# Optimization experiments

Measured on AMD Instinct MI355X. Metric: run time of the kernel, lower is better.

Reference implementation:

```python
import jax, jax.numpy as jnp
import numpy as np
from jax import lax

TWN_THRESHOLD_FACTOR = 0.05
BN_EPS = 1e-5


@jax.custom_vjp
def _ternary_quant(w, t):
    return (w > t).astype(w.dtype) - (w < -t).astype(w.dtype)

def _tq_fwd(w, t):
    mask = (w > t) | (w < -t)
    return _ternary_quant(w, t), mask

def _tq_bwd(mask, g):
    return (g * mask.astype(g.dtype), jnp.zeros((), g.dtype))

_ternary_quant.defvjp(_tq_fwd, _tq_bwd)


def quantize(w):
    # threshold is detached in the original (weight.detach().abs().max())
    t = TWN_THRESHOLD_FACTOR * jnp.max(jnp.abs(lax.stop_gradient(w)))
    return _ternary_quant(w, t)


def conv2d(x, w, b):
    # x: [N,C,H,W], w: [O,I,K,K], valid conv, stride 1
    y = lax.conv_general_dilated(x, w, (1, 1), 'VALID',
                                 dimension_numbers=('NCHW', 'OIHW', 'NCHW'))
    return y + b[None, :, None, None]


def maxpool2(x):
    return lax.reduce_window(x, -jnp.inf, lax.max,
                             (1, 1, 2, 2), (1, 1, 2, 2), 'VALID')


def bn2d(x, g, b):
    # training-mode batch norm over (N,H,W), biased variance
    m = jnp.mean(x, (0, 2, 3), keepdims=True)
    v = jnp.mean(jnp.square(x - m), (0, 2, 3), keepdims=True)
    return (x - m) * lax.rsqrt(v + BN_EPS) * g[None, :, None, None] + b[None, :, None, None]


def bn1d(x, g, b):
    m = jnp.mean(x, 0, keepdims=True)
    v = jnp.mean(jnp.square(x - m), 0, keepdims=True)
    return (x - m) * lax.rsqrt(v + BN_EPS) * g[None, :] + b[None, :]


def setup_inputs() -> dict:
    key = jax.random.key(0)
    ks = jax.random.split(key, 12)
    N = 4096
    inp = {
        'x': jax.random.normal(ks[0], (N, 1, 28, 28), jnp.float32),
        'w1': jax.random.normal(ks[1], (32, 1, 5, 5), jnp.float32) * 0.2,
        'b1': jnp.zeros((32,), jnp.float32),
        'g1': jnp.ones((32,), jnp.float32),
        'be1': jnp.zeros((32,), jnp.float32),
        'w2': jax.random.normal(ks[2], (64, 32, 5, 5), jnp.float32) * 0.05,
        'b2': jnp.zeros((64,), jnp.float32),
        'g2': jnp.ones((64,), jnp.float32),
        'be2': jnp.zeros((64,), jnp.float32),
        'wf1': jax.random.normal(ks[3], (512, 1024), jnp.float32) * 0.03,
        'bf1': jnp.zeros((512,), jnp.float32),
        'g3': jnp.ones((512,), jnp.float32),
        'be3': jnp.zeros((512,), jnp.float32),
        'wf2': jax.random.normal(ks[4], (10, 512), jnp.float32) * 0.04,
        'bf2': jnp.zeros((10,), jnp.float32),
    }
    return inp


def reference(x, w1, b1, g1, be1, w2, b2, g2, be2, wf1, bf1, g3, be3, wf2, bf2):
    h = jax.nn.relu(bn2d(conv2d(x, quantize(w1), b1), g1, be1))     # [N,32,24,24]
    h = maxpool2(h)                                                  # [N,32,12,12]
    h = jax.nn.relu(bn2d(conv2d(h, quantize(w2), b2), g2, be2))     # [N,64,8,8]
    h = maxpool2(h)                                                  # [N,64,4,4]
    h = h.reshape(h.shape[0], -1)                                    # [N,1024]
    h = jax.nn.relu(bn1d(h @ quantize(wf1).T + bf1, g3, be3))       # [N,512]
    return h @ quantize(wf2).T + bf2                                 # [N,10]
```

## Files before the change

kernel.cpp:

```cpp
#include <hip/hip_runtime.h>

#define TID ((int)threadIdx.x)
typedef unsigned short u16;
typedef short short8 __attribute__((ext_vector_type(8)));
typedef float f32x4 __attribute__((ext_vector_type(4)));
typedef float v2f __attribute__((ext_vector_type(2)));

__device__ __forceinline__ u16 f2b(float f) {
    unsigned int x = __float_as_uint(f);
    return (u16)((x + 0x7fffu + ((x >> 16) & 1u)) >> 16);
}
__device__ __forceinline__ float b2f(u16 u) {
    return __uint_as_float(((unsigned int)u) << 16);
}
__device__ __forceinline__ v2f fma2(float a, v2f b, v2f c) {
    v2f av = {a, a};
    return __builtin_elementwise_fma(av, b, c);
}

static constexpr size_t OFF_QW1   = 0;
static constexpr size_t OFF_QWF2  = 3200;
static constexpr size_t OFF_TMAX  = 23680;
static constexpr size_t OFF_SUM1C = 23808;
static constexpr size_t OFF_SSQ1C = 24832;
static constexpr size_t OFF_SUM2  = 25856, OFF_SSQ2 = 26112;
static constexpr size_t OFF_SUM3  = 26368, OFF_SSQ3 = 28416;
static constexpr size_t STATS_BEG = 23680, STATS_END = 30464;
static constexpr size_t OFF_QW2C  = 30720;
static constexpr size_t OFF_QWF1C = 133120;
static constexpr size_t OFF_Y1P   = 1181696;
static constexpr size_t OFF_Y2C   = 38930432;
static constexpr size_t OFF_H2C   = 72484864;
static constexpr size_t OFF_Y3    = 80873472;

__global__ __launch_bounds__(256) void absmax_k(const float* w1, const float* w2,
                                                const float* wf1, const float* wf2,
                                                unsigned int* tmaxbits) {
    int bid = blockIdx.x;
    int b, lb, nb; const float* src; long n;
    if (bid < 1)        { b = 0; src = w1;  n = 800;    lb = bid;       nb = 1;   }
    else if (bid < 9)   { b = 1; src = w2;  n = 51200;  lb = bid - 1;   nb = 8;   }
    else if (bid < 265) { b = 2; src = wf1; n = 524288; lb = bid - 9;   nb = 256; }
    else                { b = 3; src = wf2; n = 5120;   lb = bid - 265; nb = 1;   }
    float m = 0.f;
    for (long i = (long)lb * 256 + TID; i < n; i += (long)nb * 256)
        m = fmaxf(m, fabsf(src[i]));
    __shared__ float red[256];
    red[TID] = m; __syncthreads();
    for (int s = 128; s > 0; s >>= 1) {
        if (TID < s) red[TID] = fmaxf(red[TID], red[TID + s]);
        __syncthreads();
    }
    if (TID == 0) atomicMax(&tmaxbits[b], __float_as_uint(red[0]));
}

__global__ __launch_bounds__(256) void quant_all_k(const float* w1, const float* w2,
                                                   const float* wf1, const float* wf2,
                                                   float* qw1, u16* qw2c, u16* qwf1c,
                                                   float* qwf2, const unsigned int* tmax) {
    int bid = blockIdx.x;
    if (bid < 4) {
        int i = bid * 256 + TID; if (i >= 800) return;
        float t = 0.05f * __uint_as_float(tmax[0]);
        float v = w1[i];
        qw1[i] = (v > t) ? 1.f : ((v < -t) ? -1.f : 0.f);
    } else if (bid < 204) {
        int i = (bid - 4) * 256 + TID;
        float t = 0.05f * __uint_as_float(tmax[1]);
        int ic = i & 31, oc = (i >> 5) & 63, sh = i >> 11;
        float v = w2[(oc * 32 + ic) * 25 + sh];
        qw2c[i] = f2b((v > t) ? 1.f : ((v < -t) ? -1.f : 0.f));
    } else if (bid < 2252) {
        int i = (bid - 204) * 256 + TID;
        float t = 0.05f * __uint_as_float(tmax[2]);
        float v = wf1[i];
        qwf1c[i] = f2b((v > t) ? 1.f : ((v < -t) ? -1.f : 0.f));
    } else {
        int i = (bid - 2252) * 256 + TID;
        float t = 0.05f * __uint_as_float(tmax[3]);
        float v = wf2[i];
        qwf2[i] = (v > t) ? 1.f : ((v < -t) ? -1.f : 0.f);
    }
}

__global__ __launch_bounds__(256) void conv1_fused_k(const float* __restrict__ x,
                                                     const float* __restrict__ qw1,
                                                     u16* __restrict__ y1p,
                                                     float* sum1c, float* ssq1c) {
    __shared__ float wl[800];
    __shared__ float red[4][64];
    for (int i = TID; i < 800; i += 256) wl[i] = qw1[i];
    __syncthreads();
    int p = blockIdx.x * 256 + TID;
    int cg = p & 15, half = (p >> 4) & 1;
    int pr = p >> 5;
    int py = pr % 12, n = pr / 12;
    int l = TID & 63, wv = TID >> 6;
    const float* xb = x + n * 784 + (2 * py) * 28 + half * 12;
    float patch[6][16];
    #pragma unroll
    for (int r = 0; r < 6; r++) {
        const float4* rp = reinterpret_cast<const float4*>(xb + r * 28);
        #pragma unroll
        for (int qq = 0; qq < 4; qq++) {
            float4 v = rp[qq];
            patch[r][qq * 4 + 0] = v.x; patch[r][qq * 4 + 1] = v.y;
            patch[r][qq * 4 + 2] = v.z; patch[r][qq * 4 + 3] = v.w;
        }
    }
    int c0 = cg * 2;
    v2f wp[25];
    #pragma unroll
    for (int k = 0; k < 25; k++)
        wp[k] = (v2f){wl[c0 * 25 + k], wl[(c0 + 1) * 25 + k]};
    v2f A0[12], A1[12];
    #pragma unroll
    for (int ox = 0; ox < 12; ox++) { A0[ox] = (v2f){0.f, 0.f}; A1[ox] = (v2f){0.f, 0.f}; }
    #pragma unroll
    for (int ky = 0; ky < 5; ky++)
        #pragma unroll
        for (int kx = 0; kx < 5; kx++) {
            v2f w = wp[ky * 5 + kx];
            #pragma unroll
            for (int ox = 0; ox < 12; ox++) {
                A0[ox] = fma2(patch[ky][ox + kx], w, A0[ox]);
                A1[ox] = fma2(patch[ky + 1][ox + kx], w, A1[ox]);
            }
        }
    v2f sv = {0.f, 0.f}, qv = {0.f, 0.f};
    #pragma unroll
    for (int ox = 0; ox < 12; ox++) {
        sv += A0[ox] + A1[ox];
        qv = __builtin_elementwise_fma(A0[ox], A0[ox], qv);
        qv = __builtin_elementwise_fma(A1[ox], A1[ox], qv);
    }
    float st[4] = {sv.x, sv.y, qv.x, qv.y};
    u16* base = y1p + (size_t)n * 4608 + (py * 12 + half * 6) * 32 + c0;
    #pragma unroll
    for (int j = 0; j < 6; j++) {
        v2f pm = __builtin_elementwise_max(
                     __builtin_elementwise_max(A0[2 * j], A0[2 * j + 1]),
                     __builtin_elementwise_max(A1[2 * j], A1[2 * j + 1]));
        unsigned int u = (unsigned int)f2b(pm.x) | ((unsigned int)f2b(pm.y) << 16);
        *reinterpret_cast<unsigned int*>(base + j * 32) = u;
    }
    #pragma unroll
    for (int t = 0; t < 4; t++) {
        st[t] += __shfl_xor(st[t], 16);
        st[t] += __shfl_xor(st[t], 32);
    }
    if (l < 16) {
        #pragma unroll
        for (int t = 0; t < 4; t++) red[wv][l * 4 + t] = st[t];
    }
    __syncthreads();
    if (TID < 64) {
        float v = red[0][TID] + red[1][TID] + red[2][TID] + red[3][TID];
        int t = TID & 3, ch = (TID >> 2) * 2 + (t & 1);
        float* dst = (t < 2 ? sum1c : ssq1c) + (blockIdx.x & 7) * 32 + ch;
        atomicAdd(dst, v);
    }
}

__global__ __launch_bounds__(256) void conv2_k(const u16* __restrict__ y1p,
                                               const u16* __restrict__ qw2c,
                                               u16* __restrict__ y2c,
                                               const float* sum1c, const float* ssq1c,
                                               const float* g1, const float* be1,
                                               float* sum, float* ssq) {
    __shared__ float4 hsm4[1176];
    __shared__ float scs[32], shs[32];
    char* hsraw = (char*)hsm4;
    int n0 = blockIdx.x * 8;
    int l = TID & 63, wv = TID >> 6;
    int oc0 = wv * 16;
    int lm = l & 15, lr = (l >> 3) & 1, ox = l & 7, bq = l >> 4;
    if (TID < 32) {
        float s = 0.f, q = 0.f;
        #pragma unroll
        for (int r = 0; r < 8; r++) { s += sum1c[r * 32 + TID]; q += ssq1c[r * 32 + TID]; }
        float m = s * (1.f / 2359296.f);
        float v = q * (1.f / 2359296.f) - m * m;
        float sc = g1[TID] / sqrtf(v + 1e-5f);
        scs[TID] = sc; shs[TID] = be1[TID] - m * sc;
    }
    __syncthreads();
    float scR[8], shR[8];
    {
        int b = TID & 3;
        #pragma unroll
        for (int j = 0; j < 8; j++) { scR[j] = scs[b * 8 + j]; shR[j] = shs[b * 8 + j]; }
    }
    short8 bw[25];
    #pragma unroll
    for (int sh = 0; sh < 25; sh++)
        bw[sh] = *reinterpret_cast<const short8*>(qw2c + ((size_t)sh * 64 + oc0 + lm) * 32 + bq * 8);
    int xy[5];
    #pragma unroll
    for (int kx = 0; kx < 5; kx++) {
        int xx = ox + kx;
        xy[kx] = lr * 784 + xx * 64 + (((bq + (xx >> 1)) & 3) * 16);
    }
    float sacc = 0.f, s2acc = 0.f;
    {
        const uint4* src = reinterpret_cast<const uint4*>(y1p + (size_t)n0 * 4608);
        #pragma unroll
        for (int k = 0; k < 3; k++) {
            if (k < 2 || TID < 64) {
                int i = TID + k * 256;
                int pix = i >> 2, b = i & 3;
                int y = pix / 12, xx = pix - y * 12;
                union { uint4 v; u16 u[8]; } in, out;
                in.v = src[i];
                #pragma unroll
                for (int j = 0; j < 8; j++)
                    out.u[j] = f2b(fmaxf(fmaf(b2f(in.u[j]), scR[j], shR[j]), 0.f));
                *reinterpret_cast<uint4*>(hsraw + y * 784 + xx * 64 + (((b + (xx >> 1)) & 3) * 16)) = out.v;
            }
        }
    }
    #pragma unroll 1
    for (int s = 0; s < 8; s++) {
        __syncthreads();
        if (s < 7) {
            const uint4* src = reinterpret_cast<const uint4*>(y1p + (size_t)(n0 + s + 1) * 4608);
            char* dst = hsraw + ((s + 1) & 1) * 9408;
            #pragma unroll
            for (int k = 0; k < 3; k++) {
                if (k < 2 || TID < 64) {
                    int i = TID + k * 256;
                    int pix = i >> 2, b = i & 3;
                    int y = pix / 12, xx = pix - y * 12;
                    union { uint4 v; u16 u[8]; } in, out;
                    in.v = src[i];
                    #pragma unroll
                    for (int j = 0; j < 8; j++)
                        out.u[j] = f2b(fmaxf(fmaf(b2f(in.u[j]), scR[j], shR[j]), 0.f));
                    *reinterpret_cast<uint4*>(dst + y * 784 + xx * 64 + (((b + (xx >> 1)) & 3) * 16)) = out.v;
                }
            }
        }
        const char* hb = hsraw + (s & 1) * 9408;
        f32x4 acc[4] = {{0.f,0.f,0.f,0.f},{0.f,0.f,0.f,0.f},{0.f,0.f,0.f,0.f},{0.f,0.f,0.f,0.f}};
        #pragma unroll
        for (int R = 0; R <= 10; R++) {
            short8 a[5];
            #pragma unroll
            for (int kx = 0; kx < 5; kx++)
                a[kx] = *reinterpret_cast<const short8*>(hb + xy[kx] + R * 784);
            #pragma unroll
            for (int mt = 0; mt < 4; mt++) {
                int ky = R - 2 * mt;
                if (ky < 0 || ky > 4) continue;
                #pragma unroll
                for (int kx = 0; kx < 5; kx++)
                    acc[mt] = __builtin_amdgcn_mfma_f32_16x16x32_bf16(a[kx], bw[ky * 5 + kx], acc[mt], 0, 0, 0);
            }
        }
        int n = n0 + s;
        #pragma unroll
        for (int mt = 0; mt < 4; mt++) {
            float v0 = acc[mt][0], v1 = acc[mt][1], v2 = acc[mt][2], v3 = acc[mt][3];
            sacc += v0 + v1 + v2 + v3;
            s2acc += v0 * v0 + v1 * v1 + v2 * v2 + v3 * v3;
            ushort4 u = make_ushort4(f2b(v0), f2b(v1), f2b(v2), f2b(v3));
            *reinterpret_cast<ushort4*>(y2c + (size_t)n * 4096 + (oc0 + lm) * 64 + mt * 16 + bq * 4) = u;
        }
    }
    sacc  += __shfl_xor(sacc, 16);  sacc  += __shfl_xor(sacc, 32);
    s2acc += __shfl_xor(s2acc, 16); s2acc += __shfl_xor(s2acc, 32);
    if (l < 16) { atomicAdd(&sum[oc0 + l], sacc); atomicAdd(&ssq[oc0 + l], s2acc); }
}

__global__ __launch_bounds__(256) void pool2_k(const u16* __restrict__ y2c,
                                               const float* sum2, const float* ssq2,
                                               const float* g2, const float* be2,
                                               u16* __restrict__ h2c) {
    int i = blockIdx.x * 256 + TID;
    int px = i & 3, py = (i >> 2) & 3, oc = (i >> 4) & 63, n = i >> 10;
    float m = sum2[oc] * (1.f / 262144.f);
    float v = ssq2[oc] * (1.f / 262144.f) - m * m;
    float s = g2[oc] / sqrtf(v + 1e-5f);
    float t = be2[oc] - m * s;
    size_t base = (size_t)n * 4096 + oc * 64 + (2 * py) * 8 + 2 * px;
    unsigned int u0 = *reinterpret_cast<const unsigned int*>(y2c + base);
    unsigned int u1 = *reinterpret_cast<const unsigned int*>(y2c + base + 8);
    float a = b2f((u16)u0) * s + t, b = b2f((u16)(u0 >> 16)) * s + t;
    float c = b2f((u16)u1) * s + t, d = b2f((u16)(u1 >> 16)) * s + t;
    float mm = fmaxf(fmaxf(fmaxf(fmaxf(0.f, a), b), c), d);
    h2c[i] = f2b(mm);
}

__global__ __launch_bounds__(256) void fc1_k(const u16* __restrict__ h2c,
                                             const u16* __restrict__ qwf1c,
                                             float* __restrict__ y3T,
                                             float* sum3, float* ssq3) {
    __shared__ float4 Asm[576], Bsm[576];
    u16* AsU = (u16*)Asm; u16* BsU = (u16*)Bsm;
    int m0 = blockIdx.x * 64, j0 = blockIdx.y * 64;
    int l = TID & 63, wv = TID >> 6;
    int lm = l & 15, q = l >> 4;
    int r0 = TID >> 3, c0 = TID & 7;
    f32x4 acc[4] = {{0.f,0.f,0.f,0.f},{0.f,0.f,0.f,0.f},{0.f,0.f,0.f,0.f},{0.f,0.f,0.f,0.f}};
    #pragma unroll 1
    for (int kc = 0; kc < 16; kc++) {
        int kk = kc * 64;
        if (kc) __syncthreads();
        #pragma unroll
        for (int i = 0; i < 2; i++) {
            int r = i * 32 + r0;
            *reinterpret_cast<float4*>(AsU + r * 72 + c0 * 8) =
                *reinterpret_cast<const float4*>(h2c + (size_t)(m0 + r) * 1024 + kk + c0 * 8);
            *reinterpret_cast<float4*>(BsU + r * 72 + c0 * 8) =
                *reinterpret_cast<const float4*>(qwf1c + (size_t)(j0 + r) * 1024 + kk + c0 * 8);
        }
        __syncthreads();
        #pragma unroll
        for (int half = 0; half < 2; half++) {
            short8 b = *reinterpret_cast<const short8*>(BsU + (wv * 16 + lm) * 72 + half * 32 + q * 8);
            #pragma unroll
            for (int mt = 0; mt < 4; mt++) {
                short8 a = *reinterpret_cast<const short8*>(AsU + (mt * 16 + lm) * 72 + half * 32 + q * 8);
                acc[mt] = __builtin_amdgcn_mfma_f32_16x16x32_bf16(a, b, acc[mt], 0, 0, 0);
            }
        }
    }
    float s = 0.f, s2 = 0.f;
    #pragma unroll
    for (int mt = 0; mt < 4; mt++) {
        *reinterpret_cast<f32x4*>(y3T + (size_t)(j0 + wv * 16 + lm) * 4096 + m0 + mt * 16 + q * 4) = acc[mt];
        #pragma unroll
        for (int i = 0; i < 4; i++) { float v = acc[mt][i]; s += v; s2 = fmaf(v, v, s2); }
    }
    s  += __shfl_xor(s, 16);  s  += __shfl_xor(s, 32);
    s2 += __shfl_xor(s2, 16); s2 += __shfl_xor(s2, 32);
    if (l < 16) {
        atomicAdd(&sum3[j0 + wv * 16 + l], s);
        atomicAdd(&ssq3[j0 + wv * 16 + l], s2);
    }
}

__global__ __launch_bounds__(256) void fc2_k(const float* __restrict__ y3T,
                                             const float* sum3, const float* ssq3,
                                             const float* g3, const float* be3,
                                             const float* __restrict__ qwf2,
                                             const float* bf2, float* __restrict__ out) {
    __shared__ float wlds[5120];
    __shared__ float part[15][160];
    __shared__ float sc3s[512], sh3s[512];
    for (int i = TID; i < 5120; i += 256) wlds[i] = qwf2[i];
    for (int k = TID; k < 512; k += 256) {
        float m = sum3[k] * (1.f / 4096.f);
        float v = ssq3[k] * (1.f / 4096.f) - m * m;
        float s = g3[k] / sqrtf(v + 1e-5f);
        sc3s[k] = s; sh3s[k] = be3[k] - m * s;
    }
    __syncthreads();
    int nl = TID & 15, ks = TID >> 4;
    int n = blockIdx.x * 16 + nl;
    float acc[10] = {};
    for (int k = ks * 32; k < ks * 32 + 32; k++) {
        float v = fmaxf(y3T[(size_t)k * 4096 + n] * sc3s[k] + sh3s[k], 0.f);
        #pragma unroll
        for (int o = 0; o < 10; o++) acc[o] = fmaf(v, wlds[o * 512 + k], acc[o]);
    }
    if (ks > 0) {
        #pragma unroll
        for (int o = 0; o < 10; o++) part[ks - 1][o * 16 + nl] = acc[o];
    }
    __syncthreads();
    if (ks == 0) {
        #pragma unroll
        for (int o = 0; o < 10; o++) {
            float r = acc[o] + bf2[o];
            #pragma unroll
            for (int j = 0; j < 15; j++) r += part[j][o * 16 + nl];
            out[n * 10 + o] = r;
        }
    }
}

extern "C" void kernel_launch(void* const* d_in, const int* in_sizes, int n_in,
                              void* d_out, int out_size, void* d_ws, size_t ws_size,
                              hipStream_t stream) {
    char* wsb = (char*)d_ws;
    const float* x   = (const float*)d_in[0];
    const float* w1  = (const float*)d_in[1];
    const float* g1  = (const float*)d_in[3];
    const float* be1 = (const float*)d_in[4];
    const float* w2  = (const float*)d_in[5];
    const float* g2  = (const float*)d_in[7];
    const float* be2 = (const float*)d_in[8];
    const float* wf1 = (const float*)d_in[9];
    const float* g3  = (const float*)d_in[11];
    const float* be3 = (const float*)d_in[12];
    const float* wf2 = (const float*)d_in[13];
    const float* bf2 = (const float*)d_in[14];
    float* out = (float*)d_out;

    unsigned int* tmax = (unsigned int*)(wsb + OFF_TMAX);
    float* qw1   = (float*)(wsb + OFF_QW1);
    float* qwf2  = (float*)(wsb + OFF_QWF2);
    u16*   qw2c  = (u16*)(wsb + OFF_QW2C);
    u16*   qwf1c = (u16*)(wsb + OFF_QWF1C);
    u16*   y1p   = (u16*)(wsb + OFF_Y1P);
    u16*   y2c   = (u16*)(wsb + OFF_Y2C);
    u16*   h2c   = (u16*)(wsb + OFF_H2C);
    float* y3    = (float*)(wsb + OFF_Y3);

    float* sum1c = (float*)(wsb + OFF_SUM1C); float* ssq1c = (float*)(wsb + OFF_SSQ1C);
    float* sum2  = (float*)(wsb + OFF_SUM2);  float* ssq2  = (float*)(wsb + OFF_SSQ2);
    float* sum3  = (float*)(wsb + OFF_SUM3);  float* ssq3  = (float*)(wsb + OFF_SSQ3);

    hipMemsetAsync(wsb + STATS_BEG, 0, STATS_END - STATS_BEG, stream);

    absmax_k<<<266, 256, 0, stream>>>(w1, w2, wf1, wf2, tmax);
    quant_all_k<<<2272, 256, 0, stream>>>(w1, w2, wf1, wf2, qw1, qw2c, qwf1c, qwf2, tmax);

    conv1_fused_k<<<6144, 256, 0, stream>>>(x, qw1, y1p, sum1c, ssq1c);
    conv2_k<<<512, 256, 0, stream>>>(y1p, qw2c, y2c, sum1c, ssq1c, g1, be1, sum2, ssq2);
    pool2_k<<<16384, 256, 0, stream>>>(y2c, sum2, ssq2, g2, be2, h2c);
    fc1_k<<<dim3(64, 8), 256, 0, stream>>>(h2c, qwf1c, y3, sum3, ssq3);
    fc2_k<<<256, 256, 0, stream>>>(y3, sum3, ssq3, g3, be3, qwf2, bf2, out);
}
```

Measured before the change: 235.8 us.

## Rewrite conv1 as bf16 MFMA with shifted shared-memory input copies

```diff
diff --git a/kernel.cpp b/kernel.cpp
--- a/kernel.cpp
+++ b/kernel.cpp
@@ -4,7 +4,6 @@
 typedef unsigned short u16;
 typedef short short8 __attribute__((ext_vector_type(8)));
 typedef float f32x4 __attribute__((ext_vector_type(4)));
-typedef float v2f __attribute__((ext_vector_type(2)));
 
 __device__ __forceinline__ u16 f2b(float f) {
     unsigned int x = __float_as_uint(f);
@@ -12,10 +11,6 @@
 }
 __device__ __forceinline__ float b2f(u16 u) {
     return __uint_as_float(((unsigned int)u) << 16);
-}
-__device__ __forceinline__ v2f fma2(float a, v2f b, v2f c) {
-    v2f av = {a, a};
-    return __builtin_elementwise_fma(av, b, c);
 }
 
 static constexpr size_t OFF_QW1   = 0;
@@ -87,78 +82,108 @@
                                                      const float* __restrict__ qw1,
                                                      u16* __restrict__ y1p,
                                                      float* sum1c, float* ssq1c) {
-    __shared__ float wl[800];
-    __shared__ float red[4][64];
-    for (int i = TID; i < 800; i += 256) wl[i] = qw1[i];
-    __syncthreads();
-    int p = blockIdx.x * 256 + TID;
-    int cg = p & 15, half = (p >> 4) & 1;
-    int pr = p >> 5;
-    int py = pr % 12, n = pr / 12;
-    int l = TID & 63, wv = TID >> 6;
-    const float* xb = x + n * 784 + (2 * py) * 28 + half * 12;
-    float patch[6][16];
-    #pragma unroll
-    for (int r = 0; r < 6; r++) {
-        const float4* rp = reinterpret_cast<const float4*>(xb + r * 28);
-        #pragma unroll
-        for (int qq = 0; qq < 4; qq++) {
-            float4 v = rp[qq];
-            patch[r][qq * 4 + 0] = v.x; patch[r][qq * 4 + 1] = v.y;
-            patch[r][qq * 4 + 2] = v.z; patch[r][qq * 4 + 3] = v.w;
-        }
-    }
-    int c0 = cg * 2;
-    v2f wp[25];
-    #pragma unroll
-    for (int k = 0; k < 25; k++)
-        wp[k] = (v2f){wl[c0 * 25 + k], wl[(c0 + 1) * 25 + k]};
-    v2f A0[12], A1[12];
-    #pragma unroll
-    for (int ox = 0; ox < 12; ox++) { A0[ox] = (v2f){0.f, 0.f}; A1[ox] = (v2f){0.f, 0.f}; }
-    #pragma unroll
-    for (int ky = 0; ky < 5; ky++)
-        #pragma unroll
-        for (int kx = 0; kx < 5; kx++) {
-            v2f w = wp[ky * 5 + kx];
-            #pragma unroll
-            for (int ox = 0; ox < 12; ox++) {
-                A0[ox] = fma2(patch[ky][ox + kx], w, A0[ox]);
-                A1[ox] = fma2(patch[ky + 1][ox + kx], w, A1[ox]);
+    __shared__ __align__(16) u16 xrep[4 * 896];
+    __shared__ __align__(16) u16 hmax[4 * 2880];
+    int n = blockIdx.x;
+    int l = TID & 63, w = TID >> 6;
+    int lm = l & 15, q = l >> 4;
+
+    #pragma unroll
+    for (int i = 0; i < 7; i++)
+        reinterpret_cast<unsigned int*>(xrep)[TID + i * 256] = 0u;
+    __syncthreads();
+
+    if (TID < 196) {
+        int y = TID / 7, qc = TID % 7, c0 = qc * 4;
+        float4 v = *reinterpret_cast<const float4*>(x + n * 784 + y * 28 + c0);
+        u16 h[4] = {f2b(v.x), f2b(v.y), f2b(v.z), f2b(v.w)};
+        union { uint2 u; u16 h4[4]; } pk;
+        pk.h4[0] = h[0]; pk.h4[1] = h[1]; pk.h4[2] = h[2]; pk.h4[3] = h[3];
+        *reinterpret_cast<uint2*>(xrep + y * 32 + c0) = pk.u;
+        #pragma unroll
+        for (int r = 1; r < 4; r++)
+            #pragma unroll
+            for (int e = 0; e < 4; e++)
+                if (c0 + e >= r) xrep[r * 896 + y * 32 + (c0 + e - r)] = h[e];
+    }
+
+    short8 B1[2], B2[2];
+    #pragma unroll
+    for (int c = 0; c < 2; c++) {
+        union { short8 s; u16 h[8]; } b1, b2;
+        int ch = c * 16 + lm;
+        #pragma unroll
+        for (int j = 0; j < 8; j++) {
+            float v1 = 0.f, v2 = 0.f;
+            if (j < 5) {
+                v1 = qw1[ch * 25 + q * 5 + j];
+                v2 = qw1[ch * 25 + 20 + j];
             }
-        }
-    v2f sv = {0.f, 0.f}, qv = {0.f, 0.f};
-    #pragma unroll
-    for (int ox = 0; ox < 12; ox++) {
-        sv += A0[ox] + A1[ox];
-        qv = __builtin_elementwise_fma(A0[ox], A0[ox], qv);
-        qv = __builtin_elementwise_fma(A1[ox], A1[ox], qv);
-    }
-    float st[4] = {sv.x, sv.y, qv.x, qv.y};
-    u16* base = y1p + (size_t)n * 4608 + (py * 12 + half * 6) * 32 + c0;
-    #pragma unroll
-    for (int j = 0; j < 6; j++) {
-        v2f pm = __builtin_elementwise_max(
-                     __builtin_elementwise_max(A0[2 * j], A0[2 * j + 1]),
-                     __builtin_elementwise_max(A1[2 * j], A1[2 * j + 1]));
-        unsigned int u = (unsigned int)f2b(pm.x) | ((unsigned int)f2b(pm.y) << 16);
-        *reinterpret_cast<unsigned int*>(base + j * 32) = u;
-    }
-    #pragma unroll
-    for (int t = 0; t < 4; t++) {
-        st[t] += __shfl_xor(st[t], 16);
-        st[t] += __shfl_xor(st[t], 32);
-    }
+            b1.h[j] = f2b(v1);
+            b2.h[j] = (q == 0) ? f2b(v2) : (u16)0;
+        }
+        B1[c] = b1.s; B2[c] = b2.s;
+    }
+    __syncthreads();
+
+    float sacc0 = 0.f, sacc1 = 0.f, s2acc0 = 0.f, s2acc1 = 0.f;
+    #pragma unroll
+    for (int t = 0; t < 9; t++) {
+        int pib = t * 16 + lm;
+        int oyb = pib / 24, ox = pib - oyb * 24;
+        int oy = 6 * w + oyb;
+        int r = ox & 3;
+        const u16* base = xrep + r * 896 + (ox - r);
+        union { short8 s; uint2 u[2]; } a1, a2;
+        a1.u[0] = *reinterpret_cast<const uint2*>(base + (oy + q) * 32);
+        a1.u[1] = *reinterpret_cast<const uint2*>(base + (oy + q) * 32 + 4);
+        a2.u[0] = *reinterpret_cast<const uint2*>(base + (oy + 4) * 32);
+        a2.u[1] = *reinterpret_cast<const uint2*>(base + (oy + 4) * 32 + 4);
+        int hp = t * 8 + q * 2;
+        #pragma unroll
+        for (int c = 0; c < 2; c++) {
+            f32x4 acc = {0.f, 0.f, 0.f, 0.f};
+            acc = __builtin_amdgcn_mfma_f32_16x16x32_bf16(a1.s, B1[c], acc, 0, 0, 0);
+            acc = __builtin_amdgcn_mfma_f32_16x16x32_bf16(a2.s, B2[c], acc, 0, 0, 0);
+            float v0 = acc[0], v1 = acc[1], v2 = acc[2], v3 = acc[3];
+            if (c == 0) { sacc0 += v0 + v1 + v2 + v3;
+                          s2acc0 = fmaf(v0, v0, fmaf(v1, v1, fmaf(v2, v2, fmaf(v3, v3, s2acc0)))); }
+            else        { sacc1 += v0 + v1 + v2 + v3;
+                          s2acc1 = fmaf(v0, v0, fmaf(v1, v1, fmaf(v2, v2, fmaf(v3, v3, s2acc1)))); }
+            hmax[w * 2880 + hp * 40 + c * 16 + lm]       = f2b(fmaxf(v0, v1));
+            hmax[w * 2880 + (hp + 1) * 40 + c * 16 + lm] = f2b(fmaxf(v2, v3));
+        }
+    }
+    __syncthreads();
+
+    #pragma unroll
+    for (int k = 0; k < 3; k++) {
+        int task = k * 64 + l;
+        if (task < 144) {
+            int pp = task >> 2, g = task & 3;
+            int prow = pp / 12, col = pp - prow * 12;
+            int hpe = prow * 24 + col;
+            union { uint4 v; u16 h[8]; } r0, r1, o;
+            r0.v = *reinterpret_cast<const uint4*>(hmax + w * 2880 + hpe * 40 + g * 8);
+            r1.v = *reinterpret_cast<const uint4*>(hmax + w * 2880 + (hpe + 12) * 40 + g * 8);
+            #pragma unroll
+            for (int e = 0; e < 8; e++)
+                o.h[e] = f2b(fmaxf(b2f(r0.h[e]), b2f(r1.h[e])));
+            *reinterpret_cast<uint4*>(y1p + (size_t)n * 4608 +
+                                      ((3 * w + prow) * 12 + col) * 32 + g * 8) = o.v;
+        }
+    }
+
+    sacc0  += __shfl_xor(sacc0, 16);  sacc0  += __shfl_xor(sacc0, 32);
+    sacc1  += __shfl_xor(sacc1, 16);  sacc1  += __shfl_xor(sacc1, 32);
+    s2acc0 += __shfl_xor(s2acc0, 16); s2acc0 += __shfl_xor(s2acc0, 32);
+    s2acc1 += __shfl_xor(s2acc1, 16); s2acc1 += __shfl_xor(s2acc1, 32);
     if (l < 16) {
-        #pragma unroll
-        for (int t = 0; t < 4; t++) red[wv][l * 4 + t] = st[t];
-    }
-    __syncthreads();
-    if (TID < 64) {
-        float v = red[0][TID] + red[1][TID] + red[2][TID] + red[3][TID];
-        int t = TID & 3, ch = (TID >> 2) * 2 + (t & 1);
-        float* dst = (t < 2 ? sum1c : ssq1c) + (blockIdx.x & 7) * 32 + ch;
-        atomicAdd(dst, v);
+        int slot = (blockIdx.x & 7) * 32;
+        atomicAdd(&sum1c[slot + l], sacc0);
+        atomicAdd(&sum1c[slot + 16 + l], sacc1);
+        atomicAdd(&ssq1c[slot + l], s2acc0);
+        atomicAdd(&ssq1c[slot + 16 + l], s2acc1);
     }
 }
 
@@ -417,7 +442,7 @@
     absmax_k<<<266, 256, 0, stream>>>(w1, w2, wf1, wf2, tmax);
     quant_all_k<<<2272, 256, 0, stream>>>(w1, w2, wf1, wf2, qw1, qw2c, qwf1c, qwf2, tmax);
 
-    conv1_fused_k<<<6144, 256, 0, stream>>>(x, qw1, y1p, sum1c, ssq1c);
+    conv1_fused_k<<<4096, 256, 0, stream>>>(x, qw1, y1p, sum1c, ssq1c);
     conv2_k<<<512, 256, 0, stream>>>(y1p, qw2c, y2c, sum1c, ssq1c, g1, be1, sum2, ssq2);
     pool2_k<<<16384, 256, 0, stream>>>(y2c, sum2, ssq2, g2, be2, h2c);
     fc1_k<<<dim3(64, 8), 256, 0, stream>>>(h2c, qwf1c, y3, sum3, ssq3);
```

Measured after the change: 251.8 us. +6.8%, slower.
